# Performance work log

Hardware: AMD Instinct MI355X
Metric: run time of the kernel (lower is better)

## Reference

```python
import jax, jax.numpy as jnp
import numpy as np
from jax import lax

B_, L_, D_ = 4, 3136, 256
DH, DS, DR = 256, 16, 16  # d_inner//2, d_state, dt_rank (ceil(256/16))


def _ln(x, g, b):
    m = x.mean(-1, keepdims=True)
    v = ((x - m) ** 2).mean(-1, keepdims=True)
    return (x - m) * lax.rsqrt(v + 1e-5) * g + b


def _dwconv_same(x, w):
    # x: (B, C, L), w: (C, 1, K) depthwise, padding='same', no bias
    return lax.conv_general_dilated(x, w, (1,), 'SAME',
        dimension_numbers=('NCH', 'OIH', 'NCH'), feature_group_count=x.shape[1])


def _selective_scan(u, delta, A, Bm, Cm, Dp, delta_bias):
    # u, delta: (b, d, l); A: (d, n); Bm, Cm: (b, n, l)
    delta = jax.nn.softplus(delta + delta_bias[None, :, None])
    dA = jnp.exp(jnp.einsum('bdl,dn->lbdn', delta, A))          # (l,b,d,n)
    dBu = jnp.einsum('bdl,bnl,bdl->lbdn', delta, Bm, u)          # (l,b,d,n)
    C_l = jnp.transpose(Cm, (2, 0, 1))                           # (l,b,n)
    h0 = jnp.zeros(dA.shape[1:], u.dtype)

    def step(h, inp):
        dA_t, dBu_t, C_t = inp
        h = dA_t * h + dBu_t
        return h, jnp.einsum('bdn,bn->bd', h, C_t)

    _, ys = lax.scan(step, h0, (dA, dBu, C_l))                   # ys: (l,b,d)
    return jnp.transpose(ys, (1, 2, 0)) + u * Dp[None, :, None]


def _mamba(x, in_proj_w, conv_x_w, conv_z_w, x_proj_w, dt_proj_w, dt_proj_b, A_log, Dp, out_proj_w):
    xz = jnp.einsum('bld,ed->bel', x, in_proj_w)                 # (b, 2*DH, l)
    xb, zb = xz[:, :DH], xz[:, DH:]
    xb = jax.nn.silu(_dwconv_same(xb, conv_x_w))
    zb = jax.nn.silu(_dwconv_same(zb, conv_z_w))
    x_dbl = jnp.einsum('bdl,ed->ble', xb, x_proj_w)              # (b, l, DR+2*DS)
    dt, Bm, Cm = x_dbl[..., :DR], x_dbl[..., DR:DR + DS], x_dbl[..., DR + DS:]
    delta = jnp.einsum('blr,dr->bdl', dt, dt_proj_w)             # (b, DH, l)
    Bm = jnp.transpose(Bm, (0, 2, 1))                            # (b, DS, l)
    Cm = jnp.transpose(Cm, (0, 2, 1))
    A = -jnp.exp(A_log)
    y = _selective_scan(xb, delta, A, Bm, Cm, Dp, dt_proj_b)     # (b, DH, l)
    y = jnp.concatenate([y, zb], axis=1)                         # (b, 2*DH, l)
    return jnp.einsum('bel,de->bld', y, out_proj_w)


def _block(x, ln1_g, ln1_b, ln2_g, ln2_b, in_proj_w, conv_x_w, conv_z_w,
           x_proj_w, dt_proj_w, dt_proj_b, A_log, Dp, out_proj_w,
           mlp_w1, mlp_b1, mlp_w2, mlp_b2):
    x = x + _mamba(_ln(x, ln1_g, ln1_b), in_proj_w, conv_x_w, conv_z_w,
                   x_proj_w, dt_proj_w, dt_proj_b, A_log, Dp, out_proj_w)
    h = _ln(x, ln2_g, ln2_b)
    h = jax.nn.gelu(jnp.einsum('bld,hd->blh', h, mlp_w1) + mlp_b1, approximate=False)
    return x + (jnp.einsum('blh,dh->bld', h, mlp_w2) + mlp_b2)


def setup_inputs() -> dict:
    key = jax.random.key(0)
    ks = jax.random.split(key, 12)
    f = lambda k, s, sc=0.02: jax.random.normal(k, s, dtype=jnp.float32) * sc
    dt = jnp.exp(jax.random.uniform(ks[9], (DH,), dtype=jnp.float32)
                 * (np.log(0.1) - np.log(0.001)) + np.log(0.001))
    dt = jnp.clip(dt, 1e-4)
    inv_dt = dt + jnp.log(-jnp.expm1(-dt))
    return {
        'x': jax.random.normal(ks[0], (B_, L_, D_), dtype=jnp.float32),
        'ln1_g': jnp.ones((D_,), jnp.float32), 'ln1_b': jnp.zeros((D_,), jnp.float32),
        'ln2_g': jnp.ones((D_,), jnp.float32), 'ln2_b': jnp.zeros((D_,), jnp.float32),
        'in_proj_w': f(ks[1], (2 * DH, D_)),
        'conv_x_w': f(ks[2], (DH, 1, 3), 0.1),
        'conv_z_w': f(ks[3], (DH, 1, 3), 0.1),
        'x_proj_w': f(ks[4], (DR + 2 * DS, DH)),
        'dt_proj_w': f(ks[5], (DH, DR), DR ** -0.5),
        'dt_proj_b': inv_dt,
        'A_log': jnp.log(jnp.tile(jnp.arange(1, DS + 1, dtype=jnp.float32)[None, :], (DH, 1))),
        'Dp': jnp.ones((DH,), jnp.float32),
        'out_proj_w': f(ks[6], (D_, 2 * DH)),
        'mlp_w1': f(ks[7], (4 * D_, D_)), 'mlp_b1': jnp.zeros((4 * D_,), jnp.float32),
        'mlp_w2': f(ks[8], (D_, 4 * D_)), 'mlp_b2': jnp.zeros((D_,), jnp.float32),
    }


def reference(x, ln1_g, ln1_b, ln2_g, ln2_b, in_proj_w, conv_x_w, conv_z_w,
              x_proj_w, dt_proj_w, dt_proj_b, A_log, Dp, out_proj_w,
              mlp_w1, mlp_b1, mlp_w2, mlp_b2):
    return _block(x, ln1_g, ln1_b, ln2_g, ln2_b, in_proj_w, conv_x_w, conv_z_w,
                  x_proj_w, dt_proj_w, dt_proj_b, A_log, Dp, out_proj_w,
                  mlp_w1, mlp_b1, mlp_w2, mlp_b2)
```

## Files before the change

kernel.cpp:

```cpp
#include <hip/hip_runtime.h>
#include <hip/hip_bf16.h>

#define B_ 4
#define L_ 3136
#define D_ 256
#define NCH 49
#define LCH 64
#define M_ (B_*L_)

__device__ __forceinline__ float bf2f(unsigned short u) {
    union { unsigned int i; float f; } v; v.i = ((unsigned int)u) << 16; return v.f;
}
__device__ __forceinline__ unsigned short f2bs(float f) {
    __hip_bfloat16 h = __float2bfloat16(f);
    return *(unsigned short*)&h;
}
__device__ __forceinline__ float ldw(const void* p, size_t i, bool bf) {
    return bf ? bf2f(((const unsigned short*)p)[i]) : ((const float*)p)[i];
}
__device__ __forceinline__ void cvt4(ushort4 a, float* o) {
    o[0] = bf2f(a.x); o[1] = bf2f(a.y); o[2] = bf2f(a.z); o[3] = bf2f(a.w);
}
__device__ __forceinline__ float dpp_add_xor1(float x) {
    int m = __builtin_amdgcn_update_dpp(0, __float_as_int(x), 0xB1, 0xF, 0xF, true);
    return x + __int_as_float(m);
}
__device__ __forceinline__ float dpp_add_xor2(float x) {
    int m = __builtin_amdgcn_update_dpp(0, __float_as_int(x), 0x4E, 0xF, 0xF, true);
    return x + __int_as_float(m);
}

__global__ __launch_bounds__(256) void detect_kernel(
    const unsigned int* __restrict__ xw, int* __restrict__ flag)
{
    int t = threadIdx.x; int cnt = 0;
    for (int i = t; i < 2048; i += 256) {
        unsigned int lo = xw[i] & 0xFFFFu;
        unsigned int e = (lo >> 7) & 0xFFu;
        if (e >= 0x58u && e <= 0x97u) cnt++;
    }
    #pragma unroll
    for (int o = 32; o > 0; o >>= 1) cnt += __shfl_down(cnt, o);
    __shared__ int sred[4];
    if ((t & 63) == 0) sred[t >> 6] = cnt;
    __syncthreads();
    if (t == 0) flag[0] = (sred[0] + sred[1] + sred[2] + sred[3] > 1024) ? 1 : 0;
}

__global__ __launch_bounds__(256) void ln_kernel(
    const void* __restrict__ xin, int inmode,
    const void* __restrict__ g, const void* __restrict__ bsh,
    unsigned short* __restrict__ out, const int* __restrict__ flagp)
{
    const bool wbf = (*flagp != 0);
    const bool inbf = (inmode < 0) ? wbf : true;
    int row = blockIdx.x * 4 + (threadIdx.x >> 6);
    int lane = threadIdx.x & 63;
    size_t idx = (size_t)row * 256 + lane * 4;
    float v[4];
    if (inbf) {
        ushort4 a = *(const ushort4*)((const unsigned short*)xin + idx);
        cvt4(a, v);
    } else {
        float4 a = *(const float4*)((const float*)xin + idx);
        v[0] = a.x; v[1] = a.y; v[2] = a.z; v[3] = a.w;
    }
    float s = v[0] + v[1] + v[2] + v[3];
    float s2 = v[0]*v[0] + v[1]*v[1] + v[2]*v[2] + v[3]*v[3];
    #pragma unroll
    for (int o = 32; o > 0; o >>= 1) { s += __shfl_xor(s, o); s2 += __shfl_xor(s2, o); }
    float mean = s * (1.f / 256.f);
    float var  = s2 * (1.f / 256.f) - mean * mean;
    float rs = rsqrtf(var + 1e-5f);
    ushort4 o;
    o.x = f2bs((v[0] - mean) * rs * ldw(g, lane*4+0, wbf) + ldw(bsh, lane*4+0, wbf));
    o.y = f2bs((v[1] - mean) * rs * ldw(g, lane*4+1, wbf) + ldw(bsh, lane*4+1, wbf));
    o.z = f2bs((v[2] - mean) * rs * ldw(g, lane*4+2, wbf) + ldw(bsh, lane*4+2, wbf));
    o.w = f2bs((v[3] - mean) * rs * ldw(g, lane*4+3, wbf) + ldw(bsh, lane*4+3, wbf));
    *(ushort4*)(out + idx) = o;
}

enum { EPI_NONE = 0, EPI_SP = 1, EPI_RES = 2, EPI_GELU = 3, EPI_OUT = 4 };

typedef __attribute__((ext_vector_type(8))) short bf16x8;
typedef __attribute__((ext_vector_type(4))) float f32x4;

__device__ __forceinline__ void gload_lds16(const void* g, void* l) {
    __builtin_amdgcn_global_load_lds(
        (const __attribute__((address_space(1))) unsigned int*)g,
        (__attribute__((address_space(3))) unsigned int*)l, 16, 0, 0);
}

template<int EPI>
__global__ __launch_bounds__(256) void mgemm_kernel(
    const unsigned short* __restrict__ A, const unsigned short* __restrict__ A2, int Ksplit,
    const void* __restrict__ W, void* __restrict__ Cout,
    int N, int K, int lda, int ldc,
    const void* __restrict__ bias, const void* __restrict__ resb,
    const unsigned short* __restrict__ resf, const int* __restrict__ flagp)
{
    const bool wbf = (*flagp != 0);
    __shared__ unsigned short As[2][64][64];
    __shared__ unsigned short Ws[2][64][64];
    const int tid = threadIdx.x;

    const int nwg = gridDim.x * gridDim.y;
    int bid = blockIdx.y * gridDim.x + blockIdx.x;
    int wgid = ((nwg & 7) == 0) ? ((bid & 7) * (nwg >> 3) + (bid >> 3)) : bid;
    const int bx = wgid % gridDim.x;
    const int by = wgid / gridDim.x;
    const int bm = by * 64, bn = bx * 64;

    const int l = tid & 63, wid = tid >> 6;
    const int wr = wid >> 1, wc = wid & 1;
    const int lr = l & 15;
    const int lq = l >> 4;
    const int srow = tid >> 3;
    const int sblk = ((tid & 7) ^ (srow & 7)) * 8;
    const int dcol = (tid & 7) * 8;

    f32x4 acc[2][2] = {};
    const int NT = K >> 6;

    auto stage = [&](int buf, int k0s) {
        const unsigned short* Ab; int kc;
        if (k0s < Ksplit) { Ab = A;  kc = k0s; }
        else              { Ab = A2; kc = k0s - Ksplit; }
        gload_lds16(Ab + (size_t)(bm + srow) * lda + kc + sblk,      &As[buf][srow][dcol]);
        gload_lds16(Ab + (size_t)(bm + 32 + srow) * lda + kc + sblk, &As[buf][32 + srow][dcol]);
        if (wbf) {
            const unsigned short* Wb = (const unsigned short*)W;
            gload_lds16(Wb + (size_t)(bn + srow) * K + k0s + sblk,      &Ws[buf][srow][dcol]);
            gload_lds16(Wb + (size_t)(bn + 32 + srow) * K + k0s + sblk, &Ws[buf][32 + srow][dcol]);
        } else {
            const float* Wf = (const float*)W;
            #pragma unroll
            for (int h = 0; h < 2; ++h) {
                int row = h * 32 + srow;
                const float* p = Wf + (size_t)(bn + row) * K + k0s + (tid & 7) * 8;
                float4 w0 = *(const float4*)p;
                float4 w1 = *(const float4*)(p + 4);
                ushort4 o0, o1;
                o0.x = f2bs(w0.x); o0.y = f2bs(w0.y); o0.z = f2bs(w0.z); o0.w = f2bs(w0.w);
                o1.x = f2bs(w1.x); o1.y = f2bs(w1.y); o1.z = f2bs(w1.z); o1.w = f2bs(w1.w);
                *(ushort4*)&Ws[buf][row][sblk]     = o0;
                *(ushort4*)&Ws[buf][row][sblk + 4] = o1;
            }
        }
    };

    stage(0, 0);
    asm volatile("s_waitcnt vmcnt(0)" ::: "memory");
    __syncthreads();

    int cur = 0;
    for (int kt = 0; kt < NT; ++kt) {
        if (kt + 1 < NT) stage(cur ^ 1, (kt + 1) << 6);

        bf16x8 af[2][2], bfr[2][2];
        #pragma unroll
        for (int i = 0; i < 2; ++i) {
            #pragma unroll
            for (int ks = 0; ks < 2; ++ks) {
                int ca = ((ks * 4 + lq) ^ (lr & 7)) * 8;
                af[i][ks]  = *(const bf16x8*)&As[cur][wr * 32 + i * 16 + lr][ca];
                bfr[i][ks] = *(const bf16x8*)&Ws[cur][wc * 32 + i * 16 + lr][ca];
            }
        }
        #pragma unroll
        for (int ks = 0; ks < 2; ++ks)
            #pragma unroll
            for (int i = 0; i < 2; ++i)
                #pragma unroll
                for (int j = 0; j < 2; ++j)
                    acc[i][j] = __builtin_amdgcn_mfma_f32_16x16x32_bf16(af[i][ks], bfr[j][ks], acc[i][j], 0, 0, 0);

        if (kt + 1 < NT) {
            asm volatile("s_waitcnt vmcnt(0)" ::: "memory");
            __syncthreads();
            cur ^= 1;
        }
    }

    #pragma unroll
    for (int i = 0; i < 2; ++i) {
        #pragma unroll
        for (int j = 0; j < 2; ++j) {
            const int col = bn + wc * 32 + j * 16 + lr;
            #pragma unroll
            for (int e = 0; e < 4; ++e) {
                const int row = bm + wr * 32 + i * 16 + lq * 4 + e;
                float t = acc[i][j][e];
                if (EPI == EPI_RES) {
                    t += ldw(resb, (size_t)row * 256 + col, wbf);
                } else if (EPI == EPI_GELU) {
                    t += ldw(bias, col, wbf);
                    t = 0.5f * t * (1.f + erff(t * 0.70710678118654752f));
                } else if (EPI == EPI_OUT) {
                    t += ldw(bias, col, wbf) + bf2f(resf[(size_t)row * 256 + col]);
                }
                if (EPI == EPI_OUT && !wbf) {
                    ((float*)Cout)[(size_t)row * ldc + col] = t;
                } else {
                    ((unsigned short*)Cout)[(size_t)row * ldc + col] = f2bs(t);
                }
            }
        }
    }
}

template<int EPI, bool ABF, bool CBF>
__global__ __launch_bounds__(256) void gemm_kernel(
    const void* __restrict__ A, const void* __restrict__ A2, int Ksplit,
    const void* __restrict__ W, void* __restrict__ Cout,
    int N, int K, int lda, int ldc,
    const void* __restrict__ bias, const void* __restrict__ resb,
    const unsigned short* __restrict__ resf, const int* __restrict__ flagp)
{
    const bool wbf = (*flagp != 0);
    __shared__ float As[16][132];
    __shared__ float Ws[16][132];
    const int tid = threadIdx.x;
    const int bm = blockIdx.y * 128, bn = blockIdx.x * 128;
    const int tx = tid & 15, ty = tid >> 4;
    const int lrow = tid >> 1;
    const int lk = (tid & 1) * 8;

    float acc[8][8];
    #pragma unroll
    for (int i = 0; i < 8; ++i)
        #pragma unroll
        for (int j = 0; j < 8; ++j) acc[i][j] = 0.f;

    for (int k0 = 0; k0 < K; k0 += 16) {
        float av[8];
        if (ABF) {
            const unsigned short* Ab; int kc;
            if (k0 < Ksplit) { Ab = (const unsigned short*)A;  kc = k0; }
            else             { Ab = (const unsigned short*)A2; kc = k0 - Ksplit; }
            const unsigned short* Ap = Ab + (size_t)(bm + lrow) * lda + kc + lk;
            ushort4 a0 = *(const ushort4*)Ap;
            ushort4 a1 = *(const ushort4*)(Ap + 4);
            av[0] = bf2f(a0.x); av[1] = bf2f(a0.y); av[2] = bf2f(a0.z); av[3] = bf2f(a0.w);
            av[4] = bf2f(a1.x); av[5] = bf2f(a1.y); av[6] = bf2f(a1.z); av[7] = bf2f(a1.w);
        } else {
            const float* Ap = (const float*)A + (size_t)(bm + lrow) * lda + k0 + lk;
            float4 a0 = *(const float4*)Ap;
            float4 a1 = *(const float4*)(Ap + 4);
            av[0] = a0.x; av[1] = a0.y; av[2] = a0.z; av[3] = a0.w;
            av[4] = a1.x; av[5] = a1.y; av[6] = a1.z; av[7] = a1.w;
        }
        #pragma unroll
        for (int j = 0; j < 8; ++j) As[lk + j][lrow] = av[j];

        int n = bn + lrow;
        float wv[8];
        #pragma unroll
        for (int j = 0; j < 8; ++j) wv[j] = 0.f;
        if (n < N) {
            if (wbf) {
                const unsigned short* Wp = (const unsigned short*)W + (size_t)n * K + k0 + lk;
                ushort4 w0 = *(const ushort4*)Wp;
                ushort4 w1 = *(const ushort4*)(Wp + 4);
                wv[0] = bf2f(w0.x); wv[1] = bf2f(w0.y); wv[2] = bf2f(w0.z); wv[3] = bf2f(w0.w);
                wv[4] = bf2f(w1.x); wv[5] = bf2f(w1.y); wv[6] = bf2f(w1.z); wv[7] = bf2f(w1.w);
            } else {
                const float* Wp = (const float*)W + (size_t)n * K + k0 + lk;
                float4 w0 = *(const float4*)Wp;
                float4 w1 = *(const float4*)(Wp + 4);
                wv[0] = w0.x; wv[1] = w0.y; wv[2] = w0.z; wv[3] = w0.w;
                wv[4] = w1.x; wv[5] = w1.y; wv[6] = w1.z; wv[7] = w1.w;
            }
        }
        #pragma unroll
        for (int j = 0; j < 8; ++j) Ws[lk + j][lrow] = wv[j];
        __syncthreads();

        #pragma unroll
        for (int k = 0; k < 16; ++k) {
            float a[8], b[8];
            *(float4*)&a[0] = *(const float4*)&As[k][ty * 8];
            *(float4*)&a[4] = *(const float4*)&As[k][ty * 8 + 4];
            *(float4*)&b[0] = *(const float4*)&Ws[k][tx * 8];
            *(float4*)&b[4] = *(const float4*)&Ws[k][tx * 8 + 4];
            #pragma unroll
            for (int i = 0; i < 8; ++i)
                #pragma unroll
                for (int j = 0; j < 8; ++j)
                    acc[i][j] = fmaf(a[i], b[j], acc[i][j]);
        }
        __syncthreads();
    }

    #pragma unroll
    for (int i = 0; i < 8; ++i) {
        int m = bm + ty * 8 + i;
        #pragma unroll
        for (int jq = 0; jq < 2; ++jq) {
            int ncol = bn + tx * 8 + jq * 4;
            if (ncol < N) {
                float v[4];
                #pragma unroll
                for (int j = 0; j < 4; ++j) {
                    float t = acc[i][jq * 4 + j];
                    int n = ncol + j;
                    if (EPI == EPI_SP) {
                        t += ldw(bias, n, wbf);
                        t = (t > 20.f) ? t : log1pf(__expf(t));
                    }
                    v[j] = t;
                }
                if (CBF) {
                    ushort4 o;
                    o.x = f2bs(v[0]); o.y = f2bs(v[1]); o.z = f2bs(v[2]); o.w = f2bs(v[3]);
                    *(ushort4*)((unsigned short*)Cout + (size_t)m * ldc + ncol) = o;
                } else {
                    *(float4*)((float*)Cout + (size_t)m * ldc + ncol) = *(float4*)v;
                }
            }
        }
    }
}

__global__ __launch_bounds__(256) void conv_silu_kernel(
    const unsigned short* __restrict__ xz,
    const void* __restrict__ wx, const void* __restrict__ wz,
    unsigned short* __restrict__ u, unsigned short* __restrict__ z,
    const int* __restrict__ flagp)
{
    const bool wbf = (*flagp != 0);
    int sub = threadIdx.x >> 6;
    int c4 = (threadIdx.x & 63) * 4;
    int bl = blockIdx.x * 4 + sub;
    int l = bl % L_;
    const unsigned short* r = xz + (size_t)bl * 512;
    bool hasm = (l > 0), hasp = (l < L_ - 1);
    ushort4 zz; zz.x = 0; zz.y = 0; zz.z = 0; zz.w = 0;

    float xm[4], xc[4], xp[4];
    cvt4(hasm ? *(const ushort4*)(r + c4 - 512) : zz, xm);
    cvt4(*(const ushort4*)(r + c4), xc);
    cvt4(hasp ? *(const ushort4*)(r + c4 + 512) : zz, xp);
    ushort4 uo;
    {
        float o[4];
        #pragma unroll
        for (int j = 0; j < 4; ++j) {
            int cch = c4 + j;
            float v = xm[j] * ldw(wx, 3*cch, wbf) + xc[j] * ldw(wx, 3*cch+1, wbf) + xp[j] * ldw(wx, 3*cch+2, wbf);
            o[j] = v / (1.f + __expf(-v));
        }
        uo.x = f2bs(o[0]); uo.y = f2bs(o[1]); uo.z = f2bs(o[2]); uo.w = f2bs(o[3]);
    }
    *(ushort4*)(u + (size_t)bl * 256 + c4) = uo;

    float zm[4], zc[4], zp[4];
    cvt4(hasm ? *(const ushort4*)(r + c4 - 256) : zz, zm);
    cvt4(*(const ushort4*)(r + 256 + c4), zc);
    cvt4(hasp ? *(const ushort4*)(r + 768 + c4) : zz, zp);
    ushort4 zo;
    {
        float o[4];
        #pragma unroll
        for (int j = 0; j < 4; ++j) {
            int cch = c4 + j;
            float v = zm[j] * ldw(wz, 3*cch, wbf) + zc[j] * ldw(wz, 3*cch+1, wbf) + zp[j] * ldw(wz, 3*cch+2, wbf);
            o[j] = v / (1.f + __expf(-v));
        }
        zo.x = f2bs(o[0]); zo.y = f2bs(o[1]); zo.z = f2bs(o[2]); zo.w = f2bs(o[3]);
    }
    *(ushort4*)(z + (size_t)bl * 256 + c4) = zo;
}

__global__ __launch_bounds__(256) void scan_a_kernel(
    const unsigned short* __restrict__ delta, const unsigned short* __restrict__ u,
    const float* __restrict__ xdbl, const void* __restrict__ A_log,
    float* __restrict__ hend, float* __restrict__ dsum, const int* __restrict__ flagp)
{
    const bool wbf = (*flagp != 0);
    int blk = blockIdx.x;
    int b = blk / (NCH * 16);
    int rem = blk % (NCH * 16);
    int c = rem / 16, db = rem % 16;

    __shared__ unsigned int sdu[64][16];
    __shared__ float sB[64][16];

    const unsigned short* dp = delta + (size_t)b * L_ * 256;
    const unsigned short* up = u     + (size_t)b * L_ * 256;
    const float* xd = xdbl + (size_t)b * L_ * 48;

    int r = threadIdx.x >> 2, q = (threadIdx.x & 3) * 4;
    int lrow = c * 64 + r;
    {
        ushort4 dv = *(const ushort4*)(dp + (size_t)lrow * 256 + db * 16 + q);
        ushort4 uv = *(const ushort4*)(up + (size_t)lrow * 256 + db * 16 + q);
        uint4 pk;
        pk.x = (unsigned int)dv.x | ((unsigned int)uv.x << 16);
        pk.y = (unsigned int)dv.y | ((unsigned int)uv.y << 16);
        pk.z = (unsigned int)dv.z | ((unsigned int)uv.z << 16);
        pk.w = (unsigned int)dv.w | ((unsigned int)uv.w << 16);
        *(uint4*)&sdu[r][q] = pk;
        *(float4*)&sB[r][q] = *(const float4*)(xd + (size_t)lrow * 48 + 16 + q);
    }
    __syncthreads();

    int g = threadIdx.x >> 4, n = threadIdx.x & 15;
    int d = db * 16 + g;
    float An2 = -__expf(ldw(A_log, d * 16 + n, wbf)) * 1.44269504088896f;
    float h = 0.f, s = 0.f;
    #pragma unroll 8
    for (int t2 = 0; t2 < 64; ++t2) {
        unsigned int du = sdu[t2][g];
        float ds = __uint_as_float(du << 16);
        float ut = __uint_as_float(du & 0xFFFF0000u);
        float Bn = sB[t2][n];
        float e = exp2f(ds * An2);
        h = fmaf(e, h, ds * ut * Bn);
        s += ds;
    }
    size_t pair = (size_t)b * 256 + d;
    hend[(pair * NCH + c) * 16 + n] = h;
    if (n == 0) dsum[pair * NCH + c] = s;
}

__global__ __launch_bounds__(256) void scan_b_kernel(
    const void* __restrict__ A_log, float* __restrict__ hend,
    const float* __restrict__ dsum, const int* __restrict__ flagp)
{
    const bool wbf = (*flagp != 0);
    int gid = blockIdx.x * 256 + threadIdx.x;
    int pair = gid >> 4, n = gid & 15;
    int d = pair & 255;
    float An = -__expf(ldw(A_log, d * 16 + n, wbf));
    float H = 0.f;
    #pragma unroll 7
    for (int c = 0; c < NCH; ++c) {
        size_t idx = ((size_t)pair * NCH + c) * 16 + n;
        float he = hend[idx];
        hend[idx] = H;
        H = __expf(An * dsum[(size_t)pair * NCH + c]) * H + he;
    }
}

__global__ __launch_bounds__(256) void scan_c_kernel(
    const unsigned short* __restrict__ delta, const unsigned short* __restrict__ u,
    const float* __restrict__ xdbl, const void* __restrict__ A_log,
    const void* __restrict__ Dp, const float* __restrict__ hinit,
    unsigned short* __restrict__ y, const int* __restrict__ flagp)
{
    const bool wbf = (*flagp != 0);
    int blk = blockIdx.x;
    int b = blk / (NCH * 16);
    int rem = blk % (NCH * 16);
    int c = rem / 16, db = rem % 16;

    __shared__ unsigned int sdu[64][16];
    __shared__ float sBC[64][16][2];
    __shared__ float syp[64][16][4];
    __shared__ unsigned short sy[64][16];

    const unsigned short* dp = delta + (size_t)b * L_ * 256;
    const unsigned short* up = u     + (size_t)b * L_ * 256;
    const float* xd = xdbl + (size_t)b * L_ * 48;

    int r = threadIdx.x >> 2, q = (threadIdx.x & 3) * 4;
    int lrow = c * 64 + r;
    {
        ushort4 dv = *(const ushort4*)(dp + (size_t)lrow * 256 + db * 16 + q);
        ushort4 uv = *(const ushort4*)(up + (size_t)lrow * 256 + db * 16 + q);
        uint4 pk;
        pk.x = (unsigned int)dv.x | ((unsigned int)uv.x << 16);
        pk.y = (unsigned int)dv.y | ((unsigned int)uv.y << 16);
        pk.z = (unsigned int)dv.z | ((unsigned int)uv.z << 16);
        pk.w = (unsigned int)dv.w | ((unsigned int)uv.w << 16);
        *(uint4*)&sdu[r][q] = pk;
        float4 Bv = *(const float4*)(xd + (size_t)lrow * 48 + 16 + q);
        float4 Cv = *(const float4*)(xd + (size_t)lrow * 48 + 32 + q);
        float2 p0; p0.x = Bv.x; p0.y = Cv.x; *(float2*)&sBC[r][q + 0][0] = p0;
        float2 p1; p1.x = Bv.y; p1.y = Cv.y; *(float2*)&sBC[r][q + 1][0] = p1;
        float2 p2; p2.x = Bv.z; p2.y = Cv.z; *(float2*)&sBC[r][q + 2][0] = p2;
        float2 p3; p3.x = Bv.w; p3.y = Cv.w; *(float2*)&sBC[r][q + 3][0] = p3;
    }
    __syncthreads();

    int g = threadIdx.x >> 4, n = threadIdx.x & 15;
    int d = db * 16 + g;
    float An2 = -__expf(ldw(A_log, d * 16 + n, wbf)) * 1.44269504088896f;
    size_t pair = (size_t)b * 256 + d;
    float h = hinit[(pair * NCH + c) * 16 + n];
    const bool wlane = ((n & 3) == 0);
    #pragma unroll 4
    for (int t2 = 0; t2 < 64; ++t2) {
        unsigned int du = sdu[t2][g];
        float ds = __uint_as_float(du << 16);
        float ut = __uint_as_float(du & 0xFFFF0000u);
        float2 bc = *(const float2*)&sBC[t2][n][0];
        float e = exp2f(ds * An2);
        h = fmaf(e, h, ds * ut * bc.x);
        float yp = h * bc.y;
        yp = dpp_add_xor1(yp);
        yp = dpp_add_xor2(yp);
        if (wlane) syp[t2][g][n >> 2] = yp;
    }
    __syncthreads();

    #pragma unroll
    for (int cc = 0; cc < 4; ++cc) {
        int cell = threadIdx.x + cc * 256;
        int t2 = cell >> 4, gg = cell & 15;
        float4 p = *(const float4*)&syp[t2][gg][0];
        unsigned int du = sdu[t2][gg];
        float ut = __uint_as_float(du & 0xFFFF0000u);
        float Dd = ldw(Dp, db * 16 + gg, wbf);
        sy[t2][gg] = f2bs(p.x + p.y + p.z + p.w + ut * Dd);
    }
    __syncthreads();
    *(ushort4*)(y + ((size_t)b * L_ + c * 64 + r) * 256 + db * 16 + q) = *(ushort4*)&sy[r][q];
}

extern "C" void kernel_launch(void* const* d_in, const int* in_sizes, int n_in,
                              void* d_out, int out_size, void* d_ws, size_t ws_size,
                              hipStream_t stream) {
    const void* x         = d_in[0];
    const void* ln1_g     = d_in[1];
    const void* ln1_b     = d_in[2];
    const void* ln2_g     = d_in[3];
    const void* ln2_b     = d_in[4];
    const void* in_proj_w = d_in[5];
    const void* conv_x_w  = d_in[6];
    const void* conv_z_w  = d_in[7];
    const void* x_proj_w  = d_in[8];
    const void* dt_proj_w = d_in[9];
    const void* dt_proj_b = d_in[10];
    const void* A_log     = d_in[11];
    const void* Dp        = d_in[12];
    const void* out_proj_w= d_in[13];
    const void* mlp_w1    = d_in[14];
    const void* mlp_b1    = d_in[15];
    const void* mlp_w2    = d_in[16];
    const void* mlp_b2    = d_in[17];

    float* ws = (float*)d_ws;
    unsigned short* xz    = (unsigned short*)(ws);
    unsigned short* delta = (unsigned short*)(ws);
    unsigned short* yb    = (unsigned short*)(ws + 1605632);
    float*          xdbl  = ws + 3211264;
    float*          hend  = ws + 3813376;
    float*          dsum  = ws + 4616192;
    unsigned short* hmid  = (unsigned short*)(ws);
    unsigned short* ub    = (unsigned short*)(ws + 6422528);
    unsigned short* xres  = (unsigned short*)(ws + 6422528);
    unsigned short* xnb   = (unsigned short*)(ws + 8028160);
    int*            flag  = (int*)(ws + 9633792);

    dim3 blk(256);
    const int KNOSPLIT = 1 << 30;

    detect_kernel<<<1, blk, 0, stream>>>((const unsigned int*)x, flag);

    ln_kernel<<<M_ / 4, blk, 0, stream>>>(x, -1, ln1_g, ln1_b, xnb, flag);

    mgemm_kernel<EPI_NONE><<<dim3(8, 196), blk, 0, stream>>>(
        xnb, nullptr, KNOSPLIT, in_proj_w, xz, 512, 256, 256, 512, nullptr, nullptr, nullptr, flag);

    conv_silu_kernel<<<M_ / 4, blk, 0, stream>>>(xz, conv_x_w, conv_z_w, ub, xnb, flag);

    gemm_kernel<EPI_NONE, true, false><<<dim3(1, 98), blk, 0, stream>>>(
        ub, nullptr, 256, x_proj_w, xdbl, 48, 256, 256, 48, nullptr, nullptr, nullptr, flag);

    gemm_kernel<EPI_SP, false, true><<<dim3(2, 98), blk, 0, stream>>>(
        xdbl, nullptr, 16, dt_proj_w, delta, 256, 16, 48, 256, dt_proj_b, nullptr, nullptr, flag);

    scan_a_kernel<<<B_ * NCH * 16, blk, 0, stream>>>(delta, ub, xdbl, A_log, hend, dsum, flag);
    scan_b_kernel<<<64, blk, 0, stream>>>(A_log, hend, dsum, flag);
    scan_c_kernel<<<B_ * NCH * 16, blk, 0, stream>>>(delta, ub, xdbl, A_log, Dp, hend, yb, flag);

    mgemm_kernel<EPI_RES><<<dim3(4, 196), blk, 0, stream>>>(
        yb, xnb, 256, out_proj_w, xres, 256, 512, 256, 256, nullptr, x, nullptr, flag);

    ln_kernel<<<M_ / 4, blk, 0, stream>>>(xres, 1, ln2_g, ln2_b, xnb, flag);

    mgemm_kernel<EPI_GELU><<<dim3(16, 196), blk, 0, stream>>>(
        xnb, nullptr, KNOSPLIT, mlp_w1, hmid, 1024, 256, 256, 1024, mlp_b1, nullptr, nullptr, flag);

    mgemm_kernel<EPI_OUT><<<dim3(4, 196), blk, 0, stream>>>(
        hmid, nullptr, KNOSPLIT, mlp_w2, d_out, 256, 1024, 1024, 256, mlp_b2, nullptr, xres, flag);
}
```

Baseline: 353.4 us.

## Replace scalar FP32 x_proj/dt_proj GEMMs with MFMA kernels and widen conv

Replaces the generic FP32 SIMT GEMM used for x_proj and dt_proj with two dedicated bf16 MFMA kernels. The x_proj kernel double-buffers direct global-to-LDS loads with a swizzled layout. The dt_proj kernel splits its fp32 input into hi/lo bf16 parts to keep precision. The conv+SiLU kernel now handles 8 channels per thread and preloads its weights into registers, which is meant to cut per-element weight loads. The cost is extra code, plus bf16 rounding of x_proj inputs and weights, which may shift numerics slightly.

```diff
diff --git a/kernel.cpp b/kernel.cpp
--- a/kernel.cpp
+++ b/kernel.cpp
@@ -20,6 +20,16 @@
 }
 __device__ __forceinline__ void cvt4(ushort4 a, float* o) {
     o[0] = bf2f(a.x); o[1] = bf2f(a.y); o[2] = bf2f(a.z); o[3] = bf2f(a.w);
+}
+__device__ __forceinline__ void cvt8g(const unsigned short* p, bool v, float* o) {
+    if (v) {
+        ushort4 a = *(const ushort4*)p;
+        ushort4 b = *(const ushort4*)(p + 4);
+        cvt4(a, o); cvt4(b, o + 4);
+    } else {
+        #pragma unroll
+        for (int i = 0; i < 8; ++i) o[i] = 0.f;
+    }
 }
 __device__ __forceinline__ float dpp_add_xor1(float x) {
     int m = __builtin_amdgcn_update_dpp(0, __float_as_int(x), 0xB1, 0xF, 0xF, true);
@@ -209,114 +219,185 @@
     }
 }
 
-template<int EPI, bool ABF, bool CBF>
-__global__ __launch_bounds__(256) void gemm_kernel(
-    const void* __restrict__ A, const void* __restrict__ A2, int Ksplit,
-    const void* __restrict__ W, void* __restrict__ Cout,
-    int N, int K, int lda, int ldc,
-    const void* __restrict__ bias, const void* __restrict__ resb,
-    const unsigned short* __restrict__ resf, const int* __restrict__ flagp)
-{
-    const bool wbf = (*flagp != 0);
-    __shared__ float As[16][132];
-    __shared__ float Ws[16][132];
+__global__ __launch_bounds__(256) void xproj_kernel(
+    const unsigned short* __restrict__ A, const void* __restrict__ W,
+    float* __restrict__ Cout, const int* __restrict__ flagp)
+{
+    const bool wbf = (*flagp != 0);
+    __shared__ unsigned short As[2][64][64];
+    __shared__ unsigned short Ws[2][64][64];
     const int tid = threadIdx.x;
-    const int bm = blockIdx.y * 128, bn = blockIdx.x * 128;
-    const int tx = tid & 15, ty = tid >> 4;
-    const int lrow = tid >> 1;
-    const int lk = (tid & 1) * 8;
-
-    float acc[8][8];
-    #pragma unroll
-    for (int i = 0; i < 8; ++i)
-        #pragma unroll
-        for (int j = 0; j < 8; ++j) acc[i][j] = 0.f;
-
-    for (int k0 = 0; k0 < K; k0 += 16) {
-        float av[8];
-        if (ABF) {
-            const unsigned short* Ab; int kc;
-            if (k0 < Ksplit) { Ab = (const unsigned short*)A;  kc = k0; }
-            else             { Ab = (const unsigned short*)A2; kc = k0 - Ksplit; }
-            const unsigned short* Ap = Ab + (size_t)(bm + lrow) * lda + kc + lk;
-            ushort4 a0 = *(const ushort4*)Ap;
-            ushort4 a1 = *(const ushort4*)(Ap + 4);
-            av[0] = bf2f(a0.x); av[1] = bf2f(a0.y); av[2] = bf2f(a0.z); av[3] = bf2f(a0.w);
-            av[4] = bf2f(a1.x); av[5] = bf2f(a1.y); av[6] = bf2f(a1.z); av[7] = bf2f(a1.w);
+    const int bm = blockIdx.y * 64;
+
+    const int l = tid & 63, wid = tid >> 6;
+    const int wr = wid >> 1, wc = wid & 1;
+    const int lr = l & 15, lq = l >> 4;
+    const int srow = tid >> 3;
+    const int sblk = ((tid & 7) ^ (srow & 7)) * 8;
+    const int dcol = (tid & 7) * 8;
+
+    {
+        ushort4 zz4; zz4.x = 0; zz4.y = 0; zz4.z = 0; zz4.w = 0;
+        int buf = tid >> 7, rr = 48 + ((tid >> 3) & 15), cc = (tid & 7) * 8;
+        *(ushort4*)&Ws[buf][rr][cc] = zz4;
+        *(ushort4*)&Ws[buf][rr][cc + 4] = zz4;
+    }
+    __syncthreads();
+
+    f32x4 acc[2][2] = {};
+
+    auto stage = [&](int buf, int k0s) {
+        gload_lds16(A + (size_t)(bm + srow) * 256 + k0s + sblk,      &As[buf][srow][dcol]);
+        gload_lds16(A + (size_t)(bm + 32 + srow) * 256 + k0s + sblk, &As[buf][32 + srow][dcol]);
+        if (wbf) {
+            const unsigned short* Wb = (const unsigned short*)W;
+            gload_lds16(Wb + (size_t)srow * 256 + k0s + sblk, &Ws[buf][srow][dcol]);
+            if (srow < 16)
+                gload_lds16(Wb + (size_t)(32 + srow) * 256 + k0s + sblk, &Ws[buf][32 + srow][dcol]);
         } else {
-            const float* Ap = (const float*)A + (size_t)(bm + lrow) * lda + k0 + lk;
-            float4 a0 = *(const float4*)Ap;
-            float4 a1 = *(const float4*)(Ap + 4);
-            av[0] = a0.x; av[1] = a0.y; av[2] = a0.z; av[3] = a0.w;
-            av[4] = a1.x; av[5] = a1.y; av[6] = a1.z; av[7] = a1.w;
-        }
-        #pragma unroll
-        for (int j = 0; j < 8; ++j) As[lk + j][lrow] = av[j];
-
-        int n = bn + lrow;
-        float wv[8];
-        #pragma unroll
-        for (int j = 0; j < 8; ++j) wv[j] = 0.f;
-        if (n < N) {
-            if (wbf) {
-                const unsigned short* Wp = (const unsigned short*)W + (size_t)n * K + k0 + lk;
-                ushort4 w0 = *(const ushort4*)Wp;
-                ushort4 w1 = *(const ushort4*)(Wp + 4);
-                wv[0] = bf2f(w0.x); wv[1] = bf2f(w0.y); wv[2] = bf2f(w0.z); wv[3] = bf2f(w0.w);
-                wv[4] = bf2f(w1.x); wv[5] = bf2f(w1.y); wv[6] = bf2f(w1.z); wv[7] = bf2f(w1.w);
-            } else {
-                const float* Wp = (const float*)W + (size_t)n * K + k0 + lk;
-                float4 w0 = *(const float4*)Wp;
-                float4 w1 = *(const float4*)(Wp + 4);
-                wv[0] = w0.x; wv[1] = w0.y; wv[2] = w0.z; wv[3] = w0.w;
-                wv[4] = w1.x; wv[5] = w1.y; wv[6] = w1.z; wv[7] = w1.w;
+            const float* Wf = (const float*)W;
+            #pragma unroll
+            for (int h = 0; h < 2; ++h) {
+                int row = h * 32 + srow;
+                if (row < 48) {
+                    const float* p = Wf + (size_t)row * 256 + k0s + (tid & 7) * 8;
+                    float4 w0 = *(const float4*)p;
+                    float4 w1 = *(const float4*)(p + 4);
+                    ushort4 o0, o1;
+                    o0.x = f2bs(w0.x); o0.y = f2bs(w0.y); o0.z = f2bs(w0.z); o0.w = f2bs(w0.w);
+                    o1.x = f2bs(w1.x); o1.y = f2bs(w1.y); o1.z = f2bs(w1.z); o1.w = f2bs(w1.w);
+                    *(ushort4*)&Ws[buf][row][sblk]     = o0;
+                    *(ushort4*)&Ws[buf][row][sblk + 4] = o1;
+                }
             }
         }
-        #pragma unroll
-        for (int j = 0; j < 8; ++j) Ws[lk + j][lrow] = wv[j];
-        __syncthreads();
-
-        #pragma unroll
-        for (int k = 0; k < 16; ++k) {
-            float a[8], b[8];
-            *(float4*)&a[0] = *(const float4*)&As[k][ty * 8];
-            *(float4*)&a[4] = *(const float4*)&As[k][ty * 8 + 4];
-            *(float4*)&b[0] = *(const float4*)&Ws[k][tx * 8];
-            *(float4*)&b[4] = *(const float4*)&Ws[k][tx * 8 + 4];
-            #pragma unroll
-            for (int i = 0; i < 8; ++i)
+    };
+
+    stage(0, 0);
+    asm volatile("s_waitcnt vmcnt(0)" ::: "memory");
+    __syncthreads();
+
+    int cur = 0;
+    for (int kt = 0; kt < 4; ++kt) {
+        if (kt + 1 < 4) stage(cur ^ 1, (kt + 1) << 6);
+        bf16x8 af[2][2], bfr[2][2];
+        #pragma unroll
+        for (int i = 0; i < 2; ++i) {
+            #pragma unroll
+            for (int ks = 0; ks < 2; ++ks) {
+                int ca = ((ks * 4 + lq) ^ (lr & 7)) * 8;
+                af[i][ks]  = *(const bf16x8*)&As[cur][wr * 32 + i * 16 + lr][ca];
+                bfr[i][ks] = *(const bf16x8*)&Ws[cur][wc * 32 + i * 16 + lr][ca];
+            }
+        }
+        #pragma unroll
+        for (int ks = 0; ks < 2; ++ks)
+            #pragma unroll
+            for (int i = 0; i < 2; ++i)
                 #pragma unroll
-                for (int j = 0; j < 8; ++j)
-                    acc[i][j] = fmaf(a[i], b[j], acc[i][j]);
-        }
-        __syncthreads();
-    }
-
-    #pragma unroll
-    for (int i = 0; i < 8; ++i) {
-        int m = bm + ty * 8 + i;
-        #pragma unroll
-        for (int jq = 0; jq < 2; ++jq) {
-            int ncol = bn + tx * 8 + jq * 4;
-            if (ncol < N) {
-                float v[4];
+                for (int j = 0; j < 2; ++j)
+                    acc[i][j] = __builtin_amdgcn_mfma_f32_16x16x32_bf16(af[i][ks], bfr[j][ks], acc[i][j], 0, 0, 0);
+        if (kt + 1 < 4) {
+            asm volatile("s_waitcnt vmcnt(0)" ::: "memory");
+            __syncthreads();
+            cur ^= 1;
+        }
+    }
+
+    #pragma unroll
+    for (int i = 0; i < 2; ++i) {
+        #pragma unroll
+        for (int j = 0; j < 2; ++j) {
+            const int col = wc * 32 + j * 16 + lr;
+            if (col < 48) {
                 #pragma unroll
-                for (int j = 0; j < 4; ++j) {
-                    float t = acc[i][jq * 4 + j];
-                    int n = ncol + j;
-                    if (EPI == EPI_SP) {
-                        t += ldw(bias, n, wbf);
-                        t = (t > 20.f) ? t : log1pf(__expf(t));
-                    }
-                    v[j] = t;
+                for (int e = 0; e < 4; ++e) {
+                    const int row = bm + wr * 32 + i * 16 + lq * 4 + e;
+                    Cout[(size_t)row * 48 + col] = acc[i][j][e];
                 }
-                if (CBF) {
-                    ushort4 o;
-                    o.x = f2bs(v[0]); o.y = f2bs(v[1]); o.z = f2bs(v[2]); o.w = f2bs(v[3]);
-                    *(ushort4*)((unsigned short*)Cout + (size_t)m * ldc + ncol) = o;
-                } else {
-                    *(float4*)((float*)Cout + (size_t)m * ldc + ncol) = *(float4*)v;
-                }
+            }
+        }
+    }
+}
+
+__global__ __launch_bounds__(256) void dtgemm_kernel(
+    const float* __restrict__ Axd, const void* __restrict__ W,
+    unsigned short* __restrict__ Cout, const void* __restrict__ bias,
+    const int* __restrict__ flagp)
+{
+    const bool wbf = (*flagp != 0);
+    __shared__ unsigned short Ah[64][16];
+    __shared__ unsigned short Al[64][16];
+    __shared__ unsigned short Wb[64][16];
+    const int tid = threadIdx.x;
+    const int nwg = gridDim.x * gridDim.y;
+    int bid = blockIdx.y * gridDim.x + blockIdx.x;
+    int wgid = ((nwg & 7) == 0) ? ((bid & 7) * (nwg >> 3) + (bid >> 3)) : bid;
+    const int bx = wgid % gridDim.x, by = wgid / gridDim.x;
+    const int bm = by * 64, bn = bx * 64;
+
+    {
+        int rr = tid >> 2, cc = (tid & 3) * 4;
+        float4 v = *(const float4*)(Axd + (size_t)(bm + rr) * 48 + cc);
+        float vv[4] = {v.x, v.y, v.z, v.w};
+        ushort4 hi4, lo4;
+        unsigned short* hp = (unsigned short*)&hi4;
+        unsigned short* lp = (unsigned short*)&lo4;
+        #pragma unroll
+        for (int j = 0; j < 4; ++j) {
+            unsigned short h = f2bs(vv[j]);
+            hp[j] = h;
+            lp[j] = f2bs(vv[j] - bf2f(h));
+        }
+        *(ushort4*)&Ah[rr][cc] = hi4;
+        *(ushort4*)&Al[rr][cc] = lo4;
+        ushort4 wb4;
+        unsigned short* wp = (unsigned short*)&wb4;
+        if (wbf) {
+            wb4 = *(const ushort4*)((const unsigned short*)W + (size_t)(bn + rr) * 16 + cc);
+        } else {
+            float4 wv = *(const float4*)((const float*)W + (size_t)(bn + rr) * 16 + cc);
+            wp[0] = f2bs(wv.x); wp[1] = f2bs(wv.y); wp[2] = f2bs(wv.z); wp[3] = f2bs(wv.w);
+        }
+        *(ushort4*)&Wb[rr][cc] = wb4;
+    }
+    __syncthreads();
+
+    const int l = tid & 63, wid = tid >> 6;
+    const int wr = wid >> 1, wc = wid & 1;
+    const int lr = l & 15, lq = l >> 4;
+
+    f32x4 acc[2][2] = {};
+    bf16x8 ah[2], al8[2], wb8[2];
+    #pragma unroll
+    for (int i = 0; i < 2; ++i) { ah[i] = bf16x8{}; al8[i] = bf16x8{}; wb8[i] = bf16x8{}; }
+    if (lq < 2) {
+        #pragma unroll
+        for (int i = 0; i < 2; ++i) {
+            ah[i]  = *(const bf16x8*)&Ah[wr * 32 + i * 16 + lr][lq * 8];
+            al8[i] = *(const bf16x8*)&Al[wr * 32 + i * 16 + lr][lq * 8];
+            wb8[i] = *(const bf16x8*)&Wb[wc * 32 + i * 16 + lr][lq * 8];
+        }
+    }
+    #pragma unroll
+    for (int i = 0; i < 2; ++i)
+        #pragma unroll
+        for (int j = 0; j < 2; ++j) {
+            acc[i][j] = __builtin_amdgcn_mfma_f32_16x16x32_bf16(ah[i],  wb8[j], acc[i][j], 0, 0, 0);
+            acc[i][j] = __builtin_amdgcn_mfma_f32_16x16x32_bf16(al8[i], wb8[j], acc[i][j], 0, 0, 0);
+        }
+
+    #pragma unroll
+    for (int i = 0; i < 2; ++i) {
+        #pragma unroll
+        for (int j = 0; j < 2; ++j) {
+            const int col = bn + wc * 32 + j * 16 + lr;
+            #pragma unroll
+            for (int e = 0; e < 4; ++e) {
+                const int row = bm + wr * 32 + i * 16 + lq * 4 + e;
+                float t = acc[i][j][e] + ldw(bias, col, wbf);
+                t = (t > 20.f) ? t : log1pf(__expf(t));
+                Cout[(size_t)row * 256 + col] = f2bs(t);
             }
         }
     }
@@ -329,47 +410,67 @@
     const int* __restrict__ flagp)
 {
     const bool wbf = (*flagp != 0);
-    int sub = threadIdx.x >> 6;
-    int c4 = (threadIdx.x & 63) * 4;
-    int bl = blockIdx.x * 4 + sub;
+    int sub = threadIdx.x >> 5;
+    int cb = (threadIdx.x & 31) * 8;
+    int bl = blockIdx.x * 8 + sub;
     int l = bl % L_;
     const unsigned short* r = xz + (size_t)bl * 512;
     bool hasm = (l > 0), hasp = (l < L_ - 1);
-    ushort4 zz; zz.x = 0; zz.y = 0; zz.z = 0; zz.w = 0;
-
-    float xm[4], xc[4], xp[4];
-    cvt4(hasm ? *(const ushort4*)(r + c4 - 512) : zz, xm);
-    cvt4(*(const ushort4*)(r + c4), xc);
-    cvt4(hasp ? *(const ushort4*)(r + c4 + 512) : zz, xp);
-    ushort4 uo;
+
+    float wxa[24], wza[24];
+    if (wbf) {
+        const unsigned short* px = (const unsigned short*)wx + 3 * cb;
+        const unsigned short* pz = (const unsigned short*)wz + 3 * cb;
+        #pragma unroll
+        for (int t = 0; t < 3; ++t) {
+            cvt4(*(const ushort4*)(px + t * 8), &wxa[t * 8]);
+            cvt4(*(const ushort4*)(px + t * 8 + 4), &wxa[t * 8 + 4]);
+            cvt4(*(const ushort4*)(pz + t * 8), &wza[t * 8]);
+            cvt4(*(const ushort4*)(pz + t * 8 + 4), &wza[t * 8 + 4]);
+        }
+    } else {
+        const float* px = (const float*)wx + 3 * cb;
+        const float* pz = (const float*)wz + 3 * cb;
+        #pragma unroll
+        for (int t = 0; t < 6; ++t) {
+            *(float4*)&wxa[t * 4] = *(const float4*)(px + t * 4);
+            *(float4*)&wza[t * 4] = *(const float4*)(pz + t * 4);
+        }
+    }
+
+    float xm[8], xc[8], xp[8];
+    cvt8g(r + cb - 512, hasm, xm);
+    cvt8g(r + cb,       true, xc);
+    cvt8g(r + cb + 512, hasp, xp);
+    ushort4 o0, o1;
     {
-        float o[4];
-        #pragma unroll
-        for (int j = 0; j < 4; ++j) {
-            int cch = c4 + j;
-            float v = xm[j] * ldw(wx, 3*cch, wbf) + xc[j] * ldw(wx, 3*cch+1, wbf) + xp[j] * ldw(wx, 3*cch+2, wbf);
-            o[j] = v / (1.f + __expf(-v));
-        }
-        uo.x = f2bs(o[0]); uo.y = f2bs(o[1]); uo.z = f2bs(o[2]); uo.w = f2bs(o[3]);
-    }
-    *(ushort4*)(u + (size_t)bl * 256 + c4) = uo;
-
-    float zm[4], zc[4], zp[4];
-    cvt4(hasm ? *(const ushort4*)(r + c4 - 256) : zz, zm);
-    cvt4(*(const ushort4*)(r + 256 + c4), zc);
-    cvt4(hasp ? *(const ushort4*)(r + 768 + c4) : zz, zp);
-    ushort4 zo;
+        unsigned short* op = (unsigned short*)&o0;
+        unsigned short* op1 = (unsigned short*)&o1;
+        #pragma unroll
+        for (int j = 0; j < 8; ++j) {
+            float v = xm[j] * wxa[3 * j] + xc[j] * wxa[3 * j + 1] + xp[j] * wxa[3 * j + 2];
+            v = v / (1.f + __expf(-v));
+            if (j < 4) op[j] = f2bs(v); else op1[j - 4] = f2bs(v);
+        }
+    }
+    *(ushort4*)(u + (size_t)bl * 256 + cb) = o0;
+    *(ushort4*)(u + (size_t)bl * 256 + cb + 4) = o1;
+
+    cvt8g(r + cb - 256,  hasm, xm);
+    cvt8g(r + 256 + cb,  true, xc);
+    cvt8g(r + 768 + cb,  hasp, xp);
     {
-        float o[4];
-        #pragma unroll
-        for (int j = 0; j < 4; ++j) {
-            int cch = c4 + j;
-            float v = zm[j] * ldw(wz, 3*cch, wbf) + zc[j] * ldw(wz, 3*cch+1, wbf) + zp[j] * ldw(wz, 3*cch+2, wbf);
-            o[j] = v / (1.f + __expf(-v));
-        }
-        zo.x = f2bs(o[0]); zo.y = f2bs(o[1]); zo.z = f2bs(o[2]); zo.w = f2bs(o[3]);
-    }
-    *(ushort4*)(z + (size_t)bl * 256 + c4) = zo;
+        unsigned short* op = (unsigned short*)&o0;
+        unsigned short* op1 = (unsigned short*)&o1;
+        #pragma unroll
+        for (int j = 0; j < 8; ++j) {
+            float v = xm[j] * wza[3 * j] + xc[j] * wza[3 * j + 1] + xp[j] * wza[3 * j + 2];
+            v = v / (1.f + __expf(-v));
+            if (j < 4) op[j] = f2bs(v); else op1[j - 4] = f2bs(v);
+        }
+    }
+    *(ushort4*)(z + (size_t)bl * 256 + cb) = o0;
+    *(ushort4*)(z + (size_t)bl * 256 + cb + 4) = o1;
 }
 
 __global__ __launch_bounds__(256) void scan_a_kernel(
@@ -564,13 +665,11 @@
     mgemm_kernel<EPI_NONE><<<dim3(8, 196), blk, 0, stream>>>(
         xnb, nullptr, KNOSPLIT, in_proj_w, xz, 512, 256, 256, 512, nullptr, nullptr, nullptr, flag);
 
-    conv_silu_kernel<<<M_ / 4, blk, 0, stream>>>(xz, conv_x_w, conv_z_w, ub, xnb, flag);
-
-    gemm_kernel<EPI_NONE, true, false><<<dim3(1, 98), blk, 0, stream>>>(
-        ub, nullptr, 256, x_proj_w, xdbl, 48, 256, 256, 48, nullptr, nullptr, nullptr, flag);
-
-    gemm_kernel<EPI_SP, false, true><<<dim3(2, 98), blk, 0, stream>>>(
-        xdbl, nullptr, 16, dt_proj_w, delta, 256, 16, 48, 256, dt_proj_b, nullptr, nullptr, flag);
+    conv_silu_kernel<<<M_ / 8, blk, 0, stream>>>(xz, conv_x_w, conv_z_w, ub, xnb, flag);
+
+    xproj_kernel<<<dim3(1, 196), blk, 0, stream>>>(ub, x_proj_w, xdbl, flag);
+
+    dtgemm_kernel<<<dim3(4, 196), blk, 0, stream>>>(xdbl, dt_proj_w, delta, dt_proj_b, flag);
 
     scan_a_kernel<<<B_ * NCH * 16, blk, 0, stream>>>(delta, ub, xdbl, A_log, hend, dsum, flag);
     scan_b_kernel<<<64, blk, 0, stream>>>(A_log, hend, dsum, flag);
```

New measurement: 297.2 us. -15.9%, faster.
